# Kernel optimization log

Measured on AMD Instinct MI355X. Metric: run time of the kernel, lower is better.

Reference implementation:

```python
import jax, jax.numpy as jnp
import numpy as np
from jax import lax

K = 3           # number of channel clusters (hard-coded in the torch forward)
KM_ITERS = 50   # fixed Lloyd iterations (stand-in for sklearn KMeans, random_state=0)

SEQ_LEN, PRED_LEN, CH, BATCH = 1024, 192, 1000, 32
LH = SEQ_LEN // 2


def _pairwise_sqdist(z, c):
    # z: [N, D], c: [K, D] -> [N, K]
    zz = jnp.sum(z * z, axis=1, keepdims=True)          # [N,1]
    cc = jnp.sum(c * c, axis=1)[None, :]                # [1,K]
    return zz - 2.0 * (z @ c.T) + cc


def kmeans_labels(z, k=K, iters=KM_ITERS):
    # Deterministic Lloyd's algorithm; init = first k rows (deterministic stand-in
    # for sklearn's k-means++ with random_state=0).
    c0 = z[:k]

    def step(c, _):
        d = _pairwise_sqdist(z, c)
        labels = jnp.argmin(d, axis=1)
        ones = jnp.ones((z.shape[0],), z.dtype)
        sums = jax.ops.segment_sum(z, labels, num_segments=k)       # [K,D]
        counts = jax.ops.segment_sum(ones, labels, num_segments=k)  # [K]
        new_c = jnp.where(counts[:, None] > 0,
                          sums / jnp.maximum(counts, 1.0)[:, None], c)
        return new_c, None

    c, _ = lax.scan(step, c0, None, length=iters)
    return jnp.argmin(_pairwise_sqdist(z, c), axis=1)   # [N] int32


def setup_inputs() -> dict:
    key = jax.random.key(0)
    ks = jax.random.split(key, 4)
    x = jax.random.normal(ks[0], (BATCH, SEQ_LEN, CH), dtype=jnp.float32)
    # stacked per-cluster expert Linears g1/g2/g3: weight [K, P, Lh], bias [K, P]
    Wg = jax.random.normal(ks[1], (K, PRED_LEN, LH), dtype=jnp.float32) * 0.02
    bg = jnp.zeros((K, PRED_LEN), dtype=jnp.float32)
    Wu = jax.random.normal(ks[2], (PRED_LEN, LH), dtype=jnp.float32) * 0.02
    bu = jnp.zeros((PRED_LEN,), dtype=jnp.float32)
    z1 = jnp.zeros((1,), dtype=jnp.float32)
    return {"x": x, "x_mark_enc": z1, "x_dec": z1, "x_mark_dec": z1,
            "Wg": Wg, "bg": bg, "Wu": Wu, "bu": bu}


def reference(x, x_mark_enc, x_dec, x_mark_dec, Wg, bg, Wu, bu):
    # instance normalization over time (torch.var is unbiased -> ddof=1)
    x_mean = jnp.mean(x, axis=1, keepdims=True)
    xc = x - x_mean
    x_var = jnp.var(xc, axis=1, keepdims=True, ddof=1) + 1e-5
    xn = xc / jnp.sqrt(x_var)

    # Haar split along time
    x1 = xn[:, 0::2, :] * 0.5
    x2 = xn[:, 1::2, :] * 0.5
    x_L = x1 + x2          # [B, Lh, N]
    x_U = x1 - x2          # [B, Lh, N]

    # channel clustering on z = x_L reshaped to [N, B*Lh]
    B, Lh, N = x_L.shape
    z = x_L.reshape(B * Lh, N).T                      # [N, B*Lh]
    labels = kmeans_labels(z)                         # [N]

    # per-cluster Linear experts expressed as per-channel gathered weights
    # (identical math to gather g_k -> g_kLinear -> scatter back)
    Wn = Wg[labels]                                   # [N, P, Lh]
    bn = bg[labels]                                   # [N, P]
    g = jnp.einsum('bln,npl->bpn', x_L, Wn) + bn.T[None]   # [B, P, N]

    xu = jnp.einsum('bln,pl->bpn', x_U, Wu) + bu[None, :, None]

    xy = xu + g
    return xy * jnp.sqrt(x_var) + x_mean
```

## Files before the change

kernel.cpp:

```cpp
#include <hip/hip_runtime.h>
#include <hip/hip_bf16.h>
#include <hip/hip_cooperative_groups.h>

namespace cg = cooperative_groups;

#define B_   32
#define L_   1024
#define LH_  512
#define CH_  1000
#define PRED_ 192
#define ITERS_ 50
#define KBL_ 16384
#define SLOTS_ 1012
#define NTILES_ 253
#define NT2_ 506
#define NTRI_ 36
#define SEG_ 16

typedef __attribute__((ext_vector_type(8))) _Float16 f16x8;
typedef __attribute__((ext_vector_type(4))) float f32x4;

__device__ inline ushort f2h(float x) {
    union { _Float16 h; ushort u; } c;
    c.h = (_Float16)x;
    return c.u;
}

__global__ __launch_bounds__(256) void k1_partial(const float* __restrict__ x,
                                                  float* __restrict__ pS,
                                                  float* __restrict__ pSS) {
    int seg = blockIdx.x;
    int b = blockIdx.y;
    int t = threadIdx.x;
    if (t >= 250) return;
    int c4 = t * 4;
    const float* xp = x + (size_t)b * L_ * CH_ + (size_t)seg * 64 * CH_ + c4;
    float4 s = {0.f, 0.f, 0.f, 0.f}, ss = {0.f, 0.f, 0.f, 0.f};
#pragma unroll 4
    for (int l = 0; l < 64; ++l) {
        float4 v = *(const float4*)(xp + (size_t)l * CH_);
        s.x += v.x; s.y += v.y; s.z += v.z; s.w += v.w;
        ss.x += v.x * v.x; ss.y += v.y * v.y; ss.z += v.z * v.z; ss.w += v.w * v.w;
    }
    size_t o = ((size_t)seg * B_ + b) * CH_ + c4;
    *(float4*)(pS + o) = s;
    *(float4*)(pSS + o) = ss;
}

__global__ __launch_bounds__(256) void k1b_reduce(const float* __restrict__ pS,
                                                  const float* __restrict__ pSS,
                                                  float* __restrict__ meanT,
                                                  float* __restrict__ sstdT,
                                                  float* __restrict__ invT) {
    int idx = blockIdx.x * 256 + threadIdx.x;
    if (idx >= B_ * CH_) return;
    int c = idx % CH_;
    int b = idx / CH_;
    float s = 0.f, ss = 0.f;
#pragma unroll
    for (int seg = 0; seg < SEG_; ++seg) {
        size_t o = ((size_t)seg * B_ + b) * CH_ + c;
        s += pS[o];
        ss += pSS[o];
    }
    float m = s * (1.0f / L_);
    float var = (ss - (float)L_ * m * m) * (1.0f / (L_ - 1)) + 1e-5f;
    float sd = sqrtf(var);
    meanT[c * B_ + b] = m;
    sstdT[c * B_ + b] = sd;
    invT[c * B_ + b] = 1.0f / sd;
}

__global__ __launch_bounds__(256) void k2_build(const float* __restrict__ x,
                                                const float* __restrict__ meanT,
                                                const float* __restrict__ invT,
                                                ushort* __restrict__ zLF,
                                                ushort* __restrict__ zUF) {
    __shared__ float Ls[32][33];
    __shared__ float Us[32][33];
    int tid = threadIdx.x;
    int tx = tid & 31, ty = tid >> 5;
    int n0 = blockIdx.x * 32;
    int lh0 = blockIdx.y * 32;
    int b = blockIdx.z;
    int n = n0 + tx;
    float m = 0.f, iv = 0.f;
    if (n < CH_) { m = meanT[n * B_ + b]; iv = invT[n * B_ + b]; }
    for (int r = 0; r < 4; ++r) {
        int lh = lh0 + ty + 8 * r;
        float v0 = 0.f, v1 = 0.f;
        if (n < CH_) {
            v0 = x[((size_t)b * L_ + 2 * lh) * CH_ + n];
            v1 = x[((size_t)b * L_ + 2 * lh + 1) * CH_ + n];
        }
        float a = (v0 - m) * iv * 0.5f;
        float c2 = (v1 - m) * iv * 0.5f;
        Ls[ty + 8 * r][tx] = a + c2;
        Us[ty + 8 * r][tx] = a - c2;
    }
    __syncthreads();
    for (int r = 0; r < 4; ++r) {
        int nl = ty + 8 * r;
        int nn = n0 + nl;
        if (nn < CH_) {
            size_t dst = (size_t)nn * KBL_ + (size_t)b * LH_ + lh0 + tx;
            zLF[dst] = f2h(Ls[tx][nl]);
            zUF[dst] = f2h(Us[tx][nl]);
        }
    }
}

__global__ __launch_bounds__(256) void k0_wprep(const float* __restrict__ Wg,
                                                const float* __restrict__ Wu,
                                                ushort* __restrict__ WF2) {
    int r = blockIdx.x;
    int p = r % PRED_;
    int tid = threadIdx.x;
#pragma unroll
    for (int i = 0; i < 4; ++i) {
        int k = i * 256 + tid;
        float w = (k < 512) ? Wg[(size_t)r * LH_ + k]
                            : Wu[(size_t)p * LH_ + (k - 512)];
        WF2[(size_t)r * 1024 + k] = f2h(w);
    }
}

#define ZSPLIT_ 16
#define KSEG_   1024
#define NT_     (KSEG_ / 32)

__global__ __launch_bounds__(256) void k3_mfma(const ushort* __restrict__ zF,
                                               float* __restrict__ gpart) {
    __shared__ __align__(16) ushort AH[128][40];
    __shared__ __align__(16) ushort BH[128][40];

    int bid = blockIdx.x;
    int xcd = bid & 7, w = bid >> 3;
    int ksl = 2 * xcd + (w >= NTRI_);
    int t = (w >= NTRI_) ? w - NTRI_ : w;
    int ti = 0, tt = t;
    while (tt >= 8 - ti) { tt -= 8 - ti; ++ti; }
    int tj = ti + tt;
    int i0 = ti * 128, j0 = tj * 128;
    int kb = ksl * KSEG_;

    int tid = threadIdx.x;
    int lane = tid & 63;
    int wid = tid >> 6;
    int wr = wid >> 1, wc = wid & 1;
    int fr = lane & 15;
    int g8 = lane >> 4;

    f32x4 acc[4][4];
#pragma unroll
    for (int m = 0; m < 4; ++m)
#pragma unroll
        for (int n = 0; n < 4; ++n) acc[m][n] = (f32x4){0.f, 0.f, 0.f, 0.f};

    int srow = tid >> 2;
    int sseg = tid & 3;

    uint4 pv[4];
    auto stage_load = [&](int kt) {
        int k0 = kb + kt * 32;
#pragma unroll
        for (int s = 0; s < 4; ++s) {
            int tile = s >> 1, rep = s & 1;
            int row = srow + rep * 64;
            int grow = ((tile == 0) ? i0 : j0) + row;
            uint4 v = {0u, 0u, 0u, 0u};
            if (grow < CH_)
                v = *(const uint4*)(zF + (size_t)grow * KBL_ + k0 + sseg * 8);
            pv[s] = v;
        }
    };
    auto stage_write = [&]() {
#pragma unroll
        for (int s = 0; s < 4; ++s) {
            int tile = s >> 1, rep = s & 1;
            int row = srow + rep * 64;
            ushort* dst = (tile == 0) ? &AH[row][sseg * 8] : &BH[row][sseg * 8];
            *(uint4*)dst = pv[s];
        }
    };

    stage_load(0);
    for (int t2 = 0; t2 < NT_; ++t2) {
        __syncthreads();
        stage_write();
        __syncthreads();
        if (t2 + 1 < NT_) stage_load(t2 + 1);

        f16x8 a[4];
#pragma unroll
        for (int m = 0; m < 4; ++m)
            a[m] = *(const f16x8*)&AH[wr * 64 + m * 16 + fr][g8 * 8];
#pragma unroll
        for (int n = 0; n < 4; ++n) {
            f16x8 bv = *(const f16x8*)&BH[wc * 64 + n * 16 + fr][g8 * 8];
#pragma unroll
            for (int m = 0; m < 4; ++m)
                acc[m][n] = __builtin_amdgcn_mfma_f32_16x16x32_f16(a[m], bv, acc[m][n], 0, 0, 0);
        }
    }

    float* gp = gpart + ((size_t)ksl * NTRI_ + t) * 16384;
#pragma unroll
    for (int m = 0; m < 4; ++m) {
        int rb = wr * 64 + m * 16 + g8 * 4;
#pragma unroll
        for (int n = 0; n < 4; ++n) {
            int c = wc * 64 + n * 16 + fr;
#pragma unroll
            for (int q = 0; q < 4; ++q)
                gp[(size_t)(rb + q) * 128 + c] = acc[m][n][q];
        }
    }
}

__global__ __launch_bounds__(256) void k3b_sym(const float* __restrict__ gpart,
                                               float* __restrict__ g) {
    int t = blockIdx.x;
    int seg = blockIdx.y;
    int ti = 0, tt = t;
    while (tt >= 8 - ti) { tt -= 8 - ti; ++ti; }
    int tj = ti + tt;
    int i0 = ti * 128, j0 = tj * 128;
    int tid = threadIdx.x;
    int e0 = seg * 4096 + tid * 16;
    int r = e0 >> 7, c0 = e0 & 127;

    float4 s[4];
#pragma unroll
    for (int j = 0; j < 4; ++j) s[j] = (float4){0.f, 0.f, 0.f, 0.f};
#pragma unroll
    for (int p = 0; p < ZSPLIT_; ++p) {
        const float* src = gpart + ((size_t)p * NTRI_ + t) * 16384 + e0;
#pragma unroll
        for (int j = 0; j < 4; ++j) {
            float4 v = *(const float4*)(src + j * 4);
            s[j].x += v.x; s[j].y += v.y; s[j].z += v.z; s[j].w += v.w;
        }
    }
    int i = i0 + r;
    if (i < CH_) {
#pragma unroll
        for (int j = 0; j < 4; ++j) {
            int jc = j0 + c0 + j * 4;
            if (jc + 3 < CH_) {
                *(float4*)(g + (size_t)i * CH_ + jc) = s[j];
            } else {
#pragma unroll
                for (int e = 0; e < 4; ++e)
                    if (jc + e < CH_) g[(size_t)i * CH_ + jc + e] = ((const float*)&s[j])[e];
            }
        }
        if (ti != tj) {
#pragma unroll
            for (int j = 0; j < 4; ++j) {
#pragma unroll
                for (int e = 0; e < 4; ++e) {
                    int jc = j0 + c0 + j * 4 + e;
                    if (jc < CH_) g[(size_t)jc * CH_ + i] = ((const float*)&s[j])[e];
                }
            }
        }
    }
}

__global__ __launch_bounds__(1024) void k4_kmeans(const float* __restrict__ g,
                                                  float* __restrict__ sbuf,
                                                  int* __restrict__ chlist,
                                                  int* __restrict__ chpos,
                                                  int* __restrict__ slabel) {
    cg::grid_group grid = cg::this_grid();
    __shared__ int   lab[1024];
    __shared__ float wred[16][3];
    __shared__ float ccS[3];
    __shared__ float ccPrev[3];
    __shared__ int   cntPrev[3];
    __shared__ int   cnt2[3];
    __shared__ int   chgS;
    __shared__ int   st[4], c2r[3];

    int tid = threadIdx.x;
    int wv = tid >> 6, ln = tid & 63;
    int bpt0 = blockIdx.x * 64;

    int lbp = (tid < 3) ? tid : 3;
    lab[tid] = lbp;
    if (tid < 3) {
        cntPrev[tid] = 1;
        ccPrev[tid] = g[(size_t)tid * CH_ + tid];
    }
    __syncthreads();

    int par = 0;
    for (int it = 1; it <= ITERS_ + 1; ++it) {
        const float* sp = sbuf + par * 3 * CH_;
        float s0 = 0.f, s1 = 0.f, s2 = 0.f;
        if (tid < CH_) {
            if (it == 1) {
                const float* gr = g + (size_t)tid * CH_;
                s0 = gr[0]; s1 = gr[1]; s2 = gr[2];
            } else {
                s0 = sp[tid * 3 + 0]; s1 = sp[tid * 3 + 1]; s2 = sp[tid * 3 + 2];
            }
        }
        float c0 = (lbp == 0) ? s0 : 0.f;
        float c1 = (lbp == 1) ? s1 : 0.f;
        float c2 = (lbp == 2) ? s2 : 0.f;
#pragma unroll
        for (int m = 1; m < 64; m <<= 1) {
            c0 += __shfl_xor(c0, m);
            c1 += __shfl_xor(c1, m);
            c2 += __shfl_xor(c2, m);
        }
        if (ln == 0) { wred[wv][0] = c0; wred[wv][1] = c1; wred[wv][2] = c2; }
        if (tid == 0) { cnt2[0] = 0; cnt2[1] = 0; cnt2[2] = 0; chgS = 0; }
        __syncthreads();
        if (tid < 3) {
            float sacc = 0.f;
#pragma unroll
            for (int w2 = 0; w2 < 16; ++w2) sacc += wred[w2][tid];
            int n = cntPrev[tid];
            float cc = (n > 0) ? sacc / (float)n : ccPrev[tid];
            ccS[tid] = cc;
            ccPrev[tid] = cc;
        }
        __syncthreads();
        float cc0 = ccS[0], cc1 = ccS[1], cc2 = ccS[2];

        int nl = lbp;
        if (tid < CH_) {
            float d0 = cc0 - 2.f * s0;
            float d1 = cc1 - 2.f * s1;
            float d2 = cc2 - 2.f * s2;
            nl = 0; float dm = d0;
            if (d1 < dm) { dm = d1; nl = 1; }
            if (d2 < dm) { dm = d2; nl = 2; }
        }
        bool act = (tid < CH_);
        unsigned long long b0 = __ballot(act && nl == 0);
        unsigned long long b1 = __ballot(act && nl == 1);
        unsigned long long b2 = __ballot(act && nl == 2);
        unsigned long long bc = __ballot(act && nl != lbp);
        if (ln == 0) {
            if (b0) atomicAdd(&cnt2[0], (int)__popcll(b0));
            if (b1) atomicAdd(&cnt2[1], (int)__popcll(b1));
            if (b2) atomicAdd(&cnt2[2], (int)__popcll(b2));
            if (bc) atomicAdd(&chgS, (int)__popcll(bc));
        }
        lab[tid] = nl;
        lbp = nl;
        __syncthreads();

        if (it == ITERS_ + 1) break;
        if (chgS == 0 && it > 1) break;

        int n0n = cnt2[0], n1n = cnt2[1], n2n = cnt2[2];
        float* sq = sbuf + (par ^ 1) * 3 * CH_;
        int i = bpt0 + (tid >> 4);
        int sub = tid & 15;
        if (i < CH_) {
            const float* gr = g + (size_t)i * CH_;
            float a0 = 0.f, a1 = 0.f, a2 = 0.f;
            for (int j = sub; j < CH_; j += 16) {
                float gv = gr[j];
                int lb = lab[j];
                a0 += (lb == 0) ? gv : 0.f;
                a1 += (lb == 1) ? gv : 0.f;
                a2 += (lb == 2) ? gv : 0.f;
            }
#pragma unroll
            for (int msk = 1; msk < 16; msk <<= 1) {
                a0 += __shfl_xor(a0, msk, 16);
                a1 += __shfl_xor(a1, msk, 16);
                a2 += __shfl_xor(a2, msk, 16);
            }
            if (sub == 0) {
                float f0, f1, f2;
                if (it == 1) { f0 = gr[0]; f1 = gr[1]; f2 = gr[2]; }
                else { f0 = sp[i * 3 + 0]; f1 = sp[i * 3 + 1]; f2 = sp[i * 3 + 2]; }
                sq[i * 3 + 0] = (n0n > 0) ? a0 / (float)n0n : f0;
                sq[i * 3 + 1] = (n1n > 0) ? a1 / (float)n1n : f1;
                sq[i * 3 + 2] = (n2n > 0) ? a2 / (float)n2n : f2;
            }
        }
        if (tid < 3) cntPrev[tid] = cnt2[tid];
        par ^= 1;
        grid.sync();
    }

    if (blockIdx.x == 0) {
        if (tid == 0) {
            st[0] = 0;
            st[1] = ((cnt2[0] + 3) >> 2) << 2;
            st[2] = st[1] + (((cnt2[1] + 3) >> 2) << 2);
            st[3] = st[2] + (((cnt2[2] + 3) >> 2) << 2);
            c2r[0] = 0; c2r[1] = 0; c2r[2] = 0;
        }
        __syncthreads();
        if (tid < SLOTS_) chlist[tid] = 0;
        if (tid < NTILES_) {
            int s = tid * 4;
            slabel[tid] = (s < st[1]) ? 0 : (s < st[2]) ? 1 : (s < st[3]) ? 2 : 0;
        }
        __syncthreads();
        if (tid < CH_) {
            int lb = lab[tid];
            int r = atomicAdd(&c2r[lb], 1);
            int slot = st[lb] + r;
            chlist[slot] = tid;
            chpos[tid] = slot;
        }
    }
}

__global__ __launch_bounds__(256) void k5_grouped(const ushort* __restrict__ zLF,
                                                  const ushort* __restrict__ zUF,
                                                  const ushort* __restrict__ WF2,
                                                  const int* __restrict__ chlist,
                                                  const int* __restrict__ slabel,
                                                  const float* __restrict__ bg,
                                                  const float* __restrict__ bu,
                                                  const float* __restrict__ meanT,
                                                  const float* __restrict__ sstdT,
                                                  float* __restrict__ outP) {
    __shared__ __align__(16) ushort ZT[64][40];
    __shared__ __align__(16) ushort WT[192][40];
    __shared__ int sch[2];

    int tile = blockIdx.x;
    int tid = threadIdx.x;
    if (tid < 2) sch[tid] = chlist[tile * 2 + tid];
    int lab = slabel[tile >> 1];
    __syncthreads();

    int lane = tid & 63, wid = tid >> 6;
    int fr = lane & 15, g8 = lane >> 4;

    int srow = tid >> 2, sseg = tid & 3;
    size_t zb = (size_t)sch[srow >> 5] * KBL_ + (size_t)(srow & 31) * LH_;
    const ushort* wbase = WF2 + (size_t)(lab * PRED_) * 1024;

    f32x4 acc[4][3];
#pragma unroll
    for (int m = 0; m < 4; ++m)
#pragma unroll
        for (int n = 0; n < 3; ++n) acc[m][n] = (f32x4){0.f, 0.f, 0.f, 0.f};

    uint4 pz, pw0, pw1, pw2;
    auto stage_load = [&](int t) {
        const ushort* zsrc = (t < 16) ? zLF : zUF;
        int ko = ((t & 15) * 32) + sseg * 8;
        pz  = *(const uint4*)(zsrc + zb + ko);
        int kw = t * 32 + sseg * 8;
        pw0 = *(const uint4*)(wbase + (size_t)srow * 1024 + kw);
        pw1 = *(const uint4*)(wbase + (size_t)(srow + 64) * 1024 + kw);
        pw2 = *(const uint4*)(wbase + (size_t)(srow + 128) * 1024 + kw);
    };
    auto stage_write = [&]() {
        *(uint4*)&ZT[srow][sseg * 8] = pz;
        *(uint4*)&WT[srow][sseg * 8] = pw0;
        *(uint4*)&WT[srow + 64][sseg * 8] = pw1;
        *(uint4*)&WT[srow + 128][sseg * 8] = pw2;
    };

    stage_load(0);
    for (int t = 0; t < 32; ++t) {
        __syncthreads();
        stage_write();
        __syncthreads();
        if (t + 1 < 32) stage_load(t + 1);

        f16x8 a[4];
#pragma unroll
        for (int m = 0; m < 4; ++m)
            a[m] = *(const f16x8*)&ZT[m * 16 + fr][g8 * 8];
#pragma unroll
        for (int nf = 0; nf < 3; ++nf) {
            f16x8 bv = *(const f16x8*)&WT[wid * 48 + nf * 16 + fr][g8 * 8];
#pragma unroll
            for (int m = 0; m < 4; ++m)
                acc[m][nf] = __builtin_amdgcn_mfma_f32_16x16x32_f16(a[m], bv, acc[m][nf], 0, 0, 0);
        }
    }

#pragma unroll
    for (int m = 0; m < 4; ++m) {
#pragma unroll
        for (int q = 0; q < 4; ++q) {
            int sb = m * 16 + g8 * 4 + q;
            int sl = sb >> 5, b = sb & 31;
            int n = sch[sl];
            float sd = sstdT[n * B_ + b], mu = meanT[n * B_ + b];
            size_t obase = ((size_t)(tile * 2 + sl) * B_ + b) * PRED_;
#pragma unroll
            for (int nf = 0; nf < 3; ++nf) {
                int p = wid * 48 + nf * 16 + fr;
                float v = acc[m][nf][q] + bg[lab * PRED_ + p] + bu[p];
                outP[obase + p] = v * sd + mu;
            }
        }
    }
}

__global__ __launch_bounds__(256) void k7_unperm(const float* __restrict__ outP,
                                                 const int* __restrict__ chpos,
                                                 float* __restrict__ out) {
    int n = blockIdx.x * 256 + threadIdx.x;
    int p0 = blockIdx.y * 32;
    int b = blockIdx.z;
    if (n >= CH_) return;
    const float* src = outP + ((size_t)chpos[n] * B_ + b) * PRED_ + p0;
    float4 v[8];
#pragma unroll
    for (int j = 0; j < 8; ++j) v[j] = *(const float4*)(src + j * 4);
#pragma unroll
    for (int j = 0; j < 8; ++j) {
#pragma unroll
        for (int e = 0; e < 4; ++e) {
            int p = p0 + j * 4 + e;
            out[((size_t)b * PRED_ + p) * CH_ + n] = ((const float*)&v[j])[e];
        }
    }
}

extern "C" void kernel_launch(void* const* d_in, const int* in_sizes, int n_in,
                              void* d_out, int out_size, void* d_ws, size_t ws_size,
                              hipStream_t stream) {
    const float* x  = (const float*)d_in[0];
    const float* Wg = (const float*)d_in[4];
    const float* bg = (const float*)d_in[5];
    const float* Wu = (const float*)d_in[6];
    const float* bu = (const float*)d_in[7];
    float* out = (float*)d_out;
    (void)in_sizes; (void)n_in; (void)out_size; (void)ws_size;

    char* ws = (char*)d_ws;
    size_t off = 0;
    auto alloc = [&](size_t bytes) {
        void* p = ws + off;
        off = (off + bytes + 255) & ~(size_t)255;
        return p;
    };
    ushort* zLF  = (ushort*)alloc((size_t)16384000 * 2);
    ushort* zUF  = (ushort*)alloc((size_t)16384000 * 2);
    float*  G    = (float*)alloc((size_t)1000000 * 4);
    ushort* WF2  = (ushort*)alloc((size_t)576 * 1024 * 2);
    float*  meanT = (float*)alloc((size_t)32000 * 4);
    float*  sstdT = (float*)alloc((size_t)32000 * 4);
    float*  invT  = (float*)alloc((size_t)32000 * 4);
    float*  pS   = (float*)alloc((size_t)SEG_ * B_ * CH_ * 4);
    float*  pSS  = (float*)alloc((size_t)SEG_ * B_ * CH_ * 4);
    float*  sbuf = (float*)alloc((size_t)2 * 3 * CH_ * 4);
    int*    chlist = (int*)alloc((size_t)SLOTS_ * 4);
    int*    chpos  = (int*)alloc((size_t)1024 * 4);
    int*    slabel = (int*)alloc((size_t)256 * 4);
    char* unionBase = (char*)alloc((size_t)ZSPLIT_ * NTRI_ * 16384 * 4);
    float* Gp   = (float*)unionBase;
    float* outP = (float*)unionBase;

    k1_partial<<<dim3(SEG_, 32), 256, 0, stream>>>(x, pS, pSS);
    k1b_reduce<<<125, 256, 0, stream>>>(pS, pSS, meanT, sstdT, invT);
    k2_build<<<dim3(32, 16, 32), 256, 0, stream>>>(x, meanT, invT, zLF, zUF);
    k0_wprep<<<576, 256, 0, stream>>>(Wg, Wu, WF2);
    k3_mfma<<<8 * NTRI_ * 2, 256, 0, stream>>>(zLF, Gp);
    k3b_sym<<<dim3(NTRI_, 4), 256, 0, stream>>>(Gp, G);
    void* args[] = { (void*)&G, (void*)&sbuf, (void*)&chlist, (void*)&chpos, (void*)&slabel };
    hipLaunchCooperativeKernel((void*)k4_kmeans, dim3(16), dim3(1024), args, 0, stream);
    k5_grouped<<<NT2_, 256, 0, stream>>>(zLF, zUF, WF2, chlist, slabel,
                                         bg, bu, meanT, sstdT, outP);
    k7_unperm<<<dim3(4, 6, 32), 256, 0, stream>>>(outP, chpos, out);
}
```

Baseline: 214.2 us.

## Cache per-block Gram rows in LDS for k-means and fuse stats/weight-prep launches

The cooperative k-means kernel now runs 32 blocks instead of 16. Each block copies its 32 rows of the channel Gram matrix into about 128 KB of shared memory once, then reads them from LDS in every Lloyd iteration instead of from global memory. Each row is now reduced by 32 lanes rather than 16. Separately, the mean/std reduction and the weight-to-fp16 conversion are merged into one launch to save a kernel launch. The large LDS allocation limits occupancy to one block per CU, and the wider grid adds more participants to each grid sync.

```diff
diff --git a/kernel.cpp b/kernel.cpp
--- a/kernel.cpp
+++ b/kernel.cpp
@@ -16,6 +16,8 @@
 #define NT2_ 506
 #define NTRI_ 36
 #define SEG_ 16
+#define KMB_ 32
+#define KMP_ 32
 
 typedef __attribute__((ext_vector_type(8))) _Float16 f16x8;
 typedef __attribute__((ext_vector_type(4))) float f32x4;
@@ -47,28 +49,45 @@
     *(float4*)(pSS + o) = ss;
 }
 
-__global__ __launch_bounds__(256) void k1b_reduce(const float* __restrict__ pS,
-                                                  const float* __restrict__ pSS,
-                                                  float* __restrict__ meanT,
-                                                  float* __restrict__ sstdT,
-                                                  float* __restrict__ invT) {
-    int idx = blockIdx.x * 256 + threadIdx.x;
-    if (idx >= B_ * CH_) return;
-    int c = idx % CH_;
-    int b = idx / CH_;
-    float s = 0.f, ss = 0.f;
-#pragma unroll
-    for (int seg = 0; seg < SEG_; ++seg) {
-        size_t o = ((size_t)seg * B_ + b) * CH_ + c;
-        s += pS[o];
-        ss += pSS[o];
-    }
-    float m = s * (1.0f / L_);
-    float var = (ss - (float)L_ * m * m) * (1.0f / (L_ - 1)) + 1e-5f;
-    float sd = sqrtf(var);
-    meanT[c * B_ + b] = m;
-    sstdT[c * B_ + b] = sd;
-    invT[c * B_ + b] = 1.0f / sd;
+__global__ __launch_bounds__(256) void k1b_wprep(const float* __restrict__ pS,
+                                                 const float* __restrict__ pSS,
+                                                 float* __restrict__ meanT,
+                                                 float* __restrict__ sstdT,
+                                                 float* __restrict__ invT,
+                                                 const float* __restrict__ Wg,
+                                                 const float* __restrict__ Wu,
+                                                 ushort* __restrict__ WF2) {
+    int bx = blockIdx.x;
+    int tid = threadIdx.x;
+    if (bx < 125) {
+        int idx = bx * 256 + tid;
+        if (idx >= B_ * CH_) return;
+        int c = idx % CH_;
+        int b = idx / CH_;
+        float s = 0.f, ss = 0.f;
+#pragma unroll
+        for (int seg = 0; seg < SEG_; ++seg) {
+            size_t o = ((size_t)seg * B_ + b) * CH_ + c;
+            s += pS[o];
+            ss += pSS[o];
+        }
+        float m = s * (1.0f / L_);
+        float var = (ss - (float)L_ * m * m) * (1.0f / (L_ - 1)) + 1e-5f;
+        float sd = sqrtf(var);
+        meanT[c * B_ + b] = m;
+        sstdT[c * B_ + b] = sd;
+        invT[c * B_ + b] = 1.0f / sd;
+    } else {
+        int r = bx - 125;
+        int p = r % PRED_;
+#pragma unroll
+        for (int i = 0; i < 4; ++i) {
+            int k = i * 256 + tid;
+            float w = (k < 512) ? Wg[(size_t)r * LH_ + k]
+                                : Wu[(size_t)p * LH_ + (k - 512)];
+            WF2[(size_t)r * 1024 + k] = f2h(w);
+        }
+    }
 }
 
 __global__ __launch_bounds__(256) void k2_build(const float* __restrict__ x,
@@ -110,21 +129,6 @@
     }
 }
 
-__global__ __launch_bounds__(256) void k0_wprep(const float* __restrict__ Wg,
-                                                const float* __restrict__ Wu,
-                                                ushort* __restrict__ WF2) {
-    int r = blockIdx.x;
-    int p = r % PRED_;
-    int tid = threadIdx.x;
-#pragma unroll
-    for (int i = 0; i < 4; ++i) {
-        int k = i * 256 + tid;
-        float w = (k < 512) ? Wg[(size_t)r * LH_ + k]
-                            : Wu[(size_t)p * LH_ + (k - 512)];
-        WF2[(size_t)r * 1024 + k] = f2h(w);
-    }
-}
-
 #define ZSPLIT_ 16
 #define KSEG_   1024
 #define NT_     (KSEG_ / 32)
@@ -274,6 +278,7 @@
                                                   int* __restrict__ chpos,
                                                   int* __restrict__ slabel) {
     cg::grid_group grid = cg::this_grid();
+    __shared__ float gl[KMP_ * CH_];
     __shared__ int   lab[1024];
     __shared__ float wred[16][3];
     __shared__ float ccS[3];
@@ -284,8 +289,18 @@
     __shared__ int   st[4], c2r[3];
 
     int tid = threadIdx.x;
-    int wv = tid >> 6, ln = tid & 63;
-    int bpt0 = blockIdx.x * 64;
+    int wv = tid >> 6, ln64 = tid & 63;
+    int bpt0 = blockIdx.x * KMP_;
+
+    {
+        int nrow = CH_ - bpt0;
+        if (nrow > KMP_) nrow = KMP_;
+        if (nrow < 0) nrow = 0;
+        int nf4 = nrow * (CH_ / 4);
+        const float4* gsrc = (const float4*)(g + (size_t)bpt0 * CH_);
+        float4* gdst = (float4*)gl;
+        for (int i = tid; i < nf4; i += 1024) gdst[i] = gsrc[i];
+    }
 
     int lbp = (tid < 3) ? tid : 3;
     lab[tid] = lbp;
@@ -316,7 +331,7 @@
             c1 += __shfl_xor(c1, m);
             c2 += __shfl_xor(c2, m);
         }
-        if (ln == 0) { wred[wv][0] = c0; wred[wv][1] = c1; wred[wv][2] = c2; }
+        if (ln64 == 0) { wred[wv][0] = c0; wred[wv][1] = c1; wred[wv][2] = c2; }
         if (tid == 0) { cnt2[0] = 0; cnt2[1] = 0; cnt2[2] = 0; chgS = 0; }
         __syncthreads();
         if (tid < 3) {
@@ -345,7 +360,7 @@
         unsigned long long b1 = __ballot(act && nl == 1);
         unsigned long long b2 = __ballot(act && nl == 2);
         unsigned long long bc = __ballot(act && nl != lbp);
-        if (ln == 0) {
+        if (ln64 == 0) {
             if (b0) atomicAdd(&cnt2[0], (int)__popcll(b0));
             if (b1) atomicAdd(&cnt2[1], (int)__popcll(b1));
             if (b2) atomicAdd(&cnt2[2], (int)__popcll(b2));
@@ -360,12 +375,13 @@
 
         int n0n = cnt2[0], n1n = cnt2[1], n2n = cnt2[2];
         float* sq = sbuf + (par ^ 1) * 3 * CH_;
-        int i = bpt0 + (tid >> 4);
-        int sub = tid & 15;
+        int pl = tid >> 5;
+        int ln = tid & 31;
+        int i = bpt0 + pl;
         if (i < CH_) {
-            const float* gr = g + (size_t)i * CH_;
+            const float* gr = gl + pl * CH_;
             float a0 = 0.f, a1 = 0.f, a2 = 0.f;
-            for (int j = sub; j < CH_; j += 16) {
+            for (int j = ln; j < CH_; j += 32) {
                 float gv = gr[j];
                 int lb = lab[j];
                 a0 += (lb == 0) ? gv : 0.f;
@@ -373,12 +389,12 @@
                 a2 += (lb == 2) ? gv : 0.f;
             }
 #pragma unroll
-            for (int msk = 1; msk < 16; msk <<= 1) {
-                a0 += __shfl_xor(a0, msk, 16);
-                a1 += __shfl_xor(a1, msk, 16);
-                a2 += __shfl_xor(a2, msk, 16);
-            }
-            if (sub == 0) {
+            for (int msk = 1; msk < 32; msk <<= 1) {
+                a0 += __shfl_xor(a0, msk, 32);
+                a1 += __shfl_xor(a1, msk, 32);
+                a2 += __shfl_xor(a2, msk, 32);
+            }
+            if (ln == 0) {
                 float f0, f1, f2;
                 if (it == 1) { f0 = gr[0]; f1 = gr[1]; f2 = gr[2]; }
                 else { f0 = sp[i * 3 + 0]; f1 = sp[i * 3 + 1]; f2 = sp[i * 3 + 2]; }
@@ -563,13 +579,12 @@
     float* outP = (float*)unionBase;
 
     k1_partial<<<dim3(SEG_, 32), 256, 0, stream>>>(x, pS, pSS);
-    k1b_reduce<<<125, 256, 0, stream>>>(pS, pSS, meanT, sstdT, invT);
+    k1b_wprep<<<125 + 576, 256, 0, stream>>>(pS, pSS, meanT, sstdT, invT, Wg, Wu, WF2);
     k2_build<<<dim3(32, 16, 32), 256, 0, stream>>>(x, meanT, invT, zLF, zUF);
-    k0_wprep<<<576, 256, 0, stream>>>(Wg, Wu, WF2);
     k3_mfma<<<8 * NTRI_ * 2, 256, 0, stream>>>(zLF, Gp);
     k3b_sym<<<dim3(NTRI_, 4), 256, 0, stream>>>(Gp, G);
     void* args[] = { (void*)&G, (void*)&sbuf, (void*)&chlist, (void*)&chpos, (void*)&slabel };
-    hipLaunchCooperativeKernel((void*)k4_kmeans, dim3(16), dim3(1024), args, 0, stream);
+    hipLaunchCooperativeKernel((void*)k4_kmeans, dim3(KMB_), dim3(1024), args, 0, stream);
     k5_grouped<<<NT2_, 256, 0, stream>>>(zLF, zUF, WF2, chlist, slabel,
                                          bg, bu, meanT, sstdT, outP);
     k7_unperm<<<dim3(4, 6, 32), 256, 0, stream>>>(outP, chpos, out);
```

After: 199.4 us. 1.07x faster.
